# Performance work log

Measured on AMD Instinct MI355X. Metric: run time of the kernel, lower is better.

## Reference

```python
import jax, jax.numpy as jnp
import numpy as np

B, T, N, P, L = 8, 96, 20000, 12, 3
D = 32          # d_model (forced by channel-count identity d_model+96 == 4*d_model)
C = 4 * D       # 128 channels inside the linearized conv layers
M = 64          # random_feature_dim
TAU = 0.25
EPS = 1e-6      # numerical_stabilizer in random_feature_map


def _proj_matrix(m, d, seed=0):
    # create_random_matrix: stacked transposed-Q blocks from QR of gaussian blocks,
    # scaled row-wise by norms of a gaussian matrix (scaling=0).
    rng = np.random.RandomState(seed)
    blocks = []
    n_full = m // d
    for _ in range(n_full):
        q, _ = np.linalg.qr(rng.randn(d, d))
        blocks.append(q.T)
    rem = m - n_full * d
    if rem:
        q, _ = np.linalg.qr(rng.randn(d, d))
        blocks.append(q.T[:rem])
    mat = np.vstack(blocks)
    mult = np.linalg.norm(rng.randn(m, d), axis=1)
    return jnp.asarray(mult[:, None] * mat, dtype=jnp.float32)


def setup_inputs() -> dict:
    key = jax.random.key(0)
    ks = jax.random.split(key, 12)
    g = lambda k, shape, s=0.05: jax.random.normal(k, shape, jnp.float32) * s
    return {
        "x": jax.random.normal(ks[0], (B, T, N), jnp.float32),
        "x_mark": jax.random.uniform(ks[1], (B, T, 2), dtype=jnp.float32),
        "node_emb": g(ks[2], (N, D), 0.1),
        "time_tab": g(ks[3], (T, D), 0.1),
        "week_tab": g(ks[4], (7, D), 0.1),
        "input_w": g(ks[5], (D, 3 * T)),
        "input_b": jnp.zeros((D,), jnp.float32),
        "w1_w": g(ks[6], (D, 3 * D)),
        "w1_b": jnp.zeros((D,), jnp.float32),
        "w2_w": g(ks[7], (D, 3 * D)),
        "w2_b": jnp.zeros((D,), jnp.float32),
        "in_w": g(ks[8], (L, C, C)),
        "in_b": jnp.zeros((L, C), jnp.float32),
        "out_w": g(ks[9], (L, C, C)),
        "out_b": jnp.zeros((L, C), jnp.float32),
        "ln_g": jnp.ones((L, C), jnp.float32),
        "ln_b": jnp.zeros((L, C), jnp.float32),
        "reg_w": g(ks[10], (P, 2 * C)),
        "reg_b": jnp.zeros((P,), jnp.float32),
        "proj": _proj_matrix(M, D, seed=0),
    }


def _rfm(data, proj, is_query):
    # FAVOR+ positive random features (head dim == 1 folded out; shapes are [B,N,d])
    d = data.shape[-1]
    data = data * (float(d) ** -0.25)            # h(x) normalizer d^{-1/4}
    ratio = 1.0 / np.sqrt(float(proj.shape[0]))
    dash = jnp.einsum('bnd,md->bnm', data, proj)
    diag = 0.5 * jnp.sum(data * data, axis=-1, keepdims=True)
    if is_query:
        stab = jnp.max(dash, axis=-1, keepdims=True)          # per-row max
    else:
        stab = jnp.max(dash, axis=(1, 2), keepdims=True)      # max over features AND nodes
    return ratio * (jnp.exp(dash - diag - stab) + EPS)


def _linear_kernel(v, phi_q, phi_k):
    # associativity trick: (phi_q (phi_k^T v)) / (phi_q (phi_k^T 1))
    kv = jnp.einsum('bnm,bnc->bmc', phi_k, v)
    num = jnp.einsum('bnm,bmc->bnc', phi_q, kv)
    den = jnp.einsum('bnm,bm->bn', phi_q, jnp.sum(phi_k, axis=1))
    return num / den[..., None]


def reference(x, x_mark, node_emb, time_tab, week_tab, input_w, input_b,
              w1_w, w1_b, w2_w, w2_b, in_w, in_b, out_w, out_b,
              ln_g, ln_b, reg_w, reg_b, proj):
    Bq, Tq, Nq = x.shape
    marks = jax.lax.stop_gradient(x_mark)
    tod_idx = jnp.clip((marks[:, -1, 0] * Tq).astype(jnp.int32), 0, Tq - 1)
    dow_idx = jnp.clip((marks[:, -1, 1] * 7.0).astype(jnp.int32), 0, 6)
    time_e = jnp.broadcast_to(time_tab[tod_idx][:, None, :], (Bq, Nq, D))
    week_e = jnp.broadcast_to(week_tab[dow_idx][:, None, :], (Bq, Nq, D))
    node_e = jnp.broadcast_to(node_emb[None], (Bq, Nq, D))

    # input embedding over the flattened (feature-major) [3*T] channel axis
    tod_f = jnp.broadcast_to(x_mark[:, :, 0:1], (Bq, Tq, Nq))
    dow_f = jnp.broadcast_to(x_mark[:, :, 1:2], (Bq, Tq, Nq))
    feat = jnp.concatenate([x, tod_f, dow_f], axis=1)          # (B, 3T, N)
    x_in = jnp.einsum('bkn,ck->bnc', feat, input_w) + input_b  # (B, N, D)

    xg = jnp.concatenate([node_e, time_e, week_e], axis=-1)        # (B,N,3D)
    h = jnp.concatenate([x_in, node_e, time_e, week_e], axis=-1)   # (B,N,4D)

    inv_sqrt_tau = 1.0 / np.sqrt(TAU)
    nv1 = (jnp.einsum('bng,cg->bnc', xg, w1_w) + w1_b) * inv_sqrt_tau
    nv2 = (jnp.einsum('bng,cg->bnc', xg, w2_w) + w2_b) * inv_sqrt_tau
    # same node vectors (hence same data-derived seed / projection) every layer
    phi_q = _rfm(nv1, proj, True)    # (B,N,M)
    phi_k = _rfm(nv2, proj, False)   # (B,N,M)

    skip = h
    for i in range(L):
        res = h
        u = jax.nn.sigmoid(h @ in_w[i].T + in_b[i]) * (h @ out_w[i].T + out_b[i])
        u = _linear_kernel(u, phi_q, phi_k)
        h = u + res
        mu = jnp.mean(h, axis=-1, keepdims=True)
        var = jnp.var(h, axis=-1, keepdims=True)
        h = (h - mu) * jax.lax.rsqrt(var + 1e-5) * ln_g[i] + ln_b[i]

    out = jnp.concatenate([skip, h], axis=-1) @ reg_w.T + reg_b  # (B,N,P)
    return jnp.swapaxes(out, 1, 2)                               # (B,P,N)
```

## Files before the change

### kernel.cpp

```cpp
#include <hip/hip_runtime.h>

typedef unsigned short u16;
typedef __attribute__((ext_vector_type(8))) __bf16 bf16x8;
typedef __attribute__((ext_vector_type(4))) float f32x4;

#define BB 8
#define TT 96
#define NN 20000
#define NP 20224
#define PP 12
#define LL 3
#define DD 32
#define CC 128
#define MM 64
#define NB3 105
#define NB5 313
#define NB1 313

constexpr float KSC  = 0.8408964152537145f;
constexpr float KSC2 = 0.7071067811865476f;

__device__ inline u16 f2bf(float f){
  unsigned u = __float_as_uint(f);
  u = (u + 0x7fffu + ((u >> 16) & 1u)) >> 16;
  return (u16)u;
}
__device__ inline float bf2f(u16 h){ return __uint_as_float(((unsigned)h) << 16); }
__device__ inline unsigned fmapu(float f){
  unsigned u = __float_as_uint(f);
  return (u & 0x80000000u) ? ~u : (u | 0x80000000u);
}
__device__ inline float funmap(unsigned u){
  return (u & 0x80000000u) ? __uint_as_float(u & 0x7fffffffu) : __uint_as_float(~u);
}
__device__ inline unsigned pk2(float a, float b){
  return (unsigned)f2bf(a) | ((unsigned)f2bf(b) << 16);
}

__global__ void k0_prep(const float* xm, const float* time_tab, const float* week_tab,
                        const float* w1w, const float* w1b, const float* w2w, const float* w2b,
                        const float* inw, const float* inb, const float* proj,
                        float* bv1, float* bv2, float* sbd1, float* sbd2,
                        float* bc1, float* bc2, float* mb, int* tod, int* dow,
                        unsigned* cmx, float* ksum, float* qmat, float* emat)
{
  __shared__ float sT[BB][DD], sWk[BB][DD];
  __shared__ float sB1[BB][DD], sB2[BB][DD];
  __shared__ float sW1G[DD][DD], sW2G[DD][DD], sPJ[MM][DD];
  __shared__ int sTod[BB], sDow[BB];
  int tid = threadIdx.x;
  ksum[tid] = 0.f;
  for (int i = tid; i < DD*DD; i += 512){
    int c = i >> 5, g = i & 31;
    sW1G[c][g] = w1w[c*96 + g];
    sW2G[c][g] = w2w[c*96 + g];
  }
  for (int i = tid; i < MM*DD; i += 512) sPJ[i >> 5][i & 31] = proj[i];
  if (tid < BB){
    float t0 = xm[(tid*TT + TT-1)*2 + 0];
    float t1 = xm[(tid*TT + TT-1)*2 + 1];
    int ti = (int)(t0 * (float)TT); ti = min(max(ti, 0), TT-1);
    int di = (int)(t1 * 7.0f);      di = min(max(di, 0), 6);
    sTod[tid] = ti; sDow[tid] = di; tod[tid] = ti; dow[tid] = di;
  }
  if (tid < MM) cmx[tid] = fmapu(-3e38f);
  __syncthreads();
  if (tid < BB*DD){
    int b = tid >> 5, g = tid & 31;
    sT[b][g]  = time_tab[sTod[b]*DD + g];
    sWk[b][g] = week_tab[sDow[b]*DD + g];
  }
  __syncthreads();
  {
    int which = tid >> 8, b = (tid >> 5) & 7, c = tid & 31;
    const float* w  = which ? w2w : w1w;
    const float* wb = which ? w2b : w1b;
    float s = wb[c];
    for (int g = 0; g < DD; g++)
      s += sT[b][g]*w[c*96 + 32 + g] + sWk[b][g]*w[c*96 + 64 + g];
    if (which){ bv2[b*DD+c] = s; sB2[b][c] = s; }
    else      { bv1[b*DD+c] = s; sB1[b][c] = s; }
  }
  __syncthreads();
  for (int e = tid; e < 2*DD*MM; e += 512){
    int set = e >> 11, g = (e >> 6) & 31, m = e & 63;
    float s = 0.f;
    if (set == 0){ for (int c = 0; c < DD; c++) s += sW1G[c][g]*sPJ[m][c]; }
    else         { for (int c = 0; c < DD; c++) s += sW2G[c][g]*sPJ[m][c]; }
    qmat[e] = KSC * s;
  }
  {
    int set = tid >> 8, g = (tid >> 3) & 31, b = tid & 7;
    float s = 0.f;
    if (set == 0){ for (int c = 0; c < DD; c++) s += sW1G[c][g]*sB1[b][c]; }
    else         { for (int c = 0; c < DD; c++) s += sW2G[c][g]*sB2[b][c]; }
    emat[tid] = KSC2 * s;
  }
  {
    int b = tid >> 6, m = tid & 63;
    float s1 = 0.f, s2 = 0.f;
    for (int c = 0; c < DD; c++){
      float p = sPJ[m][c];
      s1 += sB1[b][c]*p; s2 += sB2[b][c]*p;
    }
    sbd1[b*MM+m] = KSC * s1;
    sbd2[b*MM+m] = KSC * s2;
  }
  if (tid < 16){
    int b = tid & 7;
    float s = 0.f;
    if (tid >> 3){ for (int c = 0; c < DD; c++) s += sB2[b][c]*sB2[b][c]; bc2[b] = 0.5f*KSC2*s; }
    else         { for (int c = 0; c < DD; c++) s += sB1[b][c]*sB1[b][c]; bc1[b] = 0.5f*KSC2*s; }
  }
  if (tid < 256){
    int b = tid >> 5, c = tid & 31;
    float s = inb[c];
    for (int t = 0; t < TT; t++){
      float m0 = xm[(b*TT+t)*2+0], m1 = xm[(b*TT+t)*2+1];
      s += m0 * inw[c*288 + 96 + t] + m1 * inw[c*288 + 192 + t];
    }
    mb[b*DD+c] = s;
  }
}

__global__ __launch_bounds__(256) void k1_node(
    const float* node_emb, const float* w1w, const float* w2w,
    const float* qmat, const float* emat,
    const float* gin_w, const float* gout_w,
    float* sd1, float* sd2, float* sq1, float* sq2,
    float* cr1, float* cr2, unsigned* cmx,
    u16* wbf, float* kvz)
{
  __shared__ float sQ1[DD*MM], sQ2[DD*MM];
  __shared__ float sW1[DD*DD], sW2[DD*DD];
  __shared__ float sE[2*DD*BB];
  __shared__ unsigned sCM[MM];
  int tid = threadIdx.x;
  int gid = blockIdx.x*256 + tid;
  const int TOT = NB1*256;
  for (int i = gid; i < LL*BB*MM*CC; i += TOT) kvz[i] = 0.f;
  for (int i = gid; i < 2*LL*CC*CC; i += TOT){
    int which = i / (LL*CC*CC);
    int r = i - which*(LL*CC*CC);
    wbf[i] = f2bf((which ? gout_w : gin_w)[r]);
  }
  for (int i = tid; i < DD*MM; i += 256){ sQ1[i] = qmat[i]; sQ2[i] = qmat[DD*MM + i]; }
  for (int i = tid; i < DD*DD; i += 256){
    sW1[i] = w1w[(i>>5)*96 + (i&31)];
    sW2[i] = w2w[(i>>5)*96 + (i&31)];
  }
  for (int i = tid; i < 2*DD*BB; i += 256) sE[i] = emat[i];
  if (tid < MM) sCM[tid] = fmapu(-3e38f);
  __syncthreads();
  int r = tid >> 2, q = tid & 3;
  int n = blockIdx.x*64 + r;
  bool valid = n < NN;
  int nc = valid ? n : 0;
  float nd[DD];
  #pragma unroll
  for (int g = 0; g < DD; g += 4){
    float4 v = *(const float4*)&node_emb[nc*DD + g];
    nd[g] = v.x; nd[g+1] = v.y; nd[g+2] = v.z; nd[g+3] = v.w;
  }
  float s1v[16], s2v[16];
  #pragma unroll
  for (int j = 0; j < 16; j++){ s1v[j] = 0.f; s2v[j] = 0.f; }
  #pragma unroll
  for (int g = 0; g < DD; g++){
    float xg = nd[g];
    #pragma unroll
    for (int jj = 0; jj < 16; jj += 4){
      float4 a1 = *(const float4*)&sQ1[g*MM + q*16 + jj];
      float4 a2 = *(const float4*)&sQ2[g*MM + q*16 + jj];
      s1v[jj+0] += xg*a1.x; s1v[jj+1] += xg*a1.y; s1v[jj+2] += xg*a1.z; s1v[jj+3] += xg*a1.w;
      s2v[jj+0] += xg*a2.x; s2v[jj+1] += xg*a2.y; s2v[jj+2] += xg*a2.z; s2v[jj+3] += xg*a2.w;
    }
  }
  if (valid){
    #pragma unroll
    for (int jj = 0; jj < 16; jj += 4){
      *(float4*)&sd1[(size_t)n*MM + q*16 + jj] = make_float4(s1v[jj], s1v[jj+1], s1v[jj+2], s1v[jj+3]);
      *(float4*)&sd2[(size_t)n*MM + q*16 + jj] = make_float4(s2v[jj], s2v[jj+1], s2v[jj+2], s2v[jj+3]);
    }
    #pragma unroll
    for (int j = 0; j < 16; j++)
      atomicMax(&sCM[q*16 + j], fmapu(s2v[j]));
  }
  float sqp1 = 0.f, sqp2 = 0.f;
  #pragma unroll
  for (int c8 = 0; c8 < 8; c8++){
    int c = q*8 + c8;
    float d1 = 0.f, d2 = 0.f;
    #pragma unroll
    for (int g = 0; g < DD; g += 4){
      float4 w1v = *(const float4*)&sW1[c*DD + g];
      float4 w2v = *(const float4*)&sW2[c*DD + g];
      d1 += nd[g]*w1v.x + nd[g+1]*w1v.y + nd[g+2]*w1v.z + nd[g+3]*w1v.w;
      d2 += nd[g]*w2v.x + nd[g+1]*w2v.y + nd[g+2]*w2v.z + nd[g+3]*w2v.w;
    }
    sqp1 += d1*d1; sqp2 += d2*d2;
  }
  sqp1 += __shfl_xor(sqp1, 1); sqp1 += __shfl_xor(sqp1, 2);
  sqp2 += __shfl_xor(sqp2, 1); sqp2 += __shfl_xor(sqp2, 2);
  if (q == 0 && valid){
    sq1[n] = 0.5f*KSC2*sqp1;
    sq2[n] = 0.5f*KSC2*sqp2;
  }
  {
    float cA1 = 0.f, cB1 = 0.f, cA2 = 0.f, cB2 = 0.f;
    #pragma unroll
    for (int g = 0; g < DD; g++){
      float xg = nd[g];
      cA1 += xg*sE[g*8 + 2*q];
      cB1 += xg*sE[g*8 + 2*q + 1];
      cA2 += xg*sE[256 + g*8 + 2*q];
      cB2 += xg*sE[256 + g*8 + 2*q + 1];
    }
    if (valid){
      cr1[(2*q)*NN + n]     = cA1;
      cr1[(2*q+1)*NN + n]   = cB1;
      cr2[(2*q)*NN + n]     = cA2;
      cr2[(2*q+1)*NN + n]   = cB2;
    }
  }
  __syncthreads();
  if (tid < MM) atomicMax(&cmx[tid], sCM[tid]);
}

__global__ void k0b_stab(const unsigned* cmx, const float* sbd2, float* stab){
  int lane = threadIdx.x;
  float cm = funmap(cmx[lane]);
  for (int b = 0; b < BB; b++){
    float v = cm + sbd2[b*MM + lane];
    #pragma unroll
    for (int off = 32; off; off >>= 1) v = fmaxf(v, __shfl_xor(v, off));
    if (lane == 0) stab[b] = v;
  }
}

__global__ __launch_bounds__(256) void k1b_phi(
    const float* sd1, const float* sd2, const float* sq1, const float* sq2,
    const float* cr1, const float* cr2, const float* sbd1, const float* sbd2,
    const float* bc1, const float* bc2, const float* stab,
    u16* phiq, u16* phikt, float* ksum)
{
  __shared__ u16 sT[MM][264];
  __shared__ float sQb[MM], sKb[MM];
  __shared__ float sRed[256];
  int tid = threadIdx.x;
  int b = blockIdx.y, n0 = blockIdx.x*256;
  if (tid < MM){
    sQb[tid] = sbd1[b*MM + tid];
    sKb[tid] = sbd2[b*MM + tid] - bc2[b] - stab[b];
  }
  __syncthreads();
  int n = n0 + tid;
  bool v = n < NN;
  int nc = v ? n : 0;
  float dq[MM];
  const float* s1r = sd1 + (size_t)nc*MM;
  #pragma unroll
  for (int m = 0; m < MM; m += 4){
    float4 t = *(const float4*)&s1r[m];
    dq[m]=t.x; dq[m+1]=t.y; dq[m+2]=t.z; dq[m+3]=t.w;
  }
  float rm = -3e38f;
  #pragma unroll
  for (int m = 0; m < MM; m++) rm = fmaxf(rm, dq[m] + sQb[m]);
  float diagq = sq1[nc] + cr1[b*NN + nc] + bc1[b];
  u16* pqr = phiq + ((size_t)(b*NN) + nc)*MM;
  #pragma unroll
  for (int m = 0; m < MM; m += 8){
    float p[8];
    #pragma unroll
    for (int j = 0; j < 8; j++){
      float ev = dq[m+j] + sQb[m+j] - rm - diagq;
      p[j] = 0.125f*__expf(ev) + 1.25e-7f;
    }
    uint4 w = { pk2(p[0],p[1]), pk2(p[2],p[3]), pk2(p[4],p[5]), pk2(p[6],p[7]) };
    if (v) *(uint4*)&pqr[m] = w;
  }
  const float* s2r = sd2 + (size_t)nc*MM;
  float diagk = sq2[nc] + cr2[b*NN + nc];
  #pragma unroll
  for (int m = 0; m < MM; m++){
    float ev = s2r[m] + sKb[m] - diagk;
    float pv = v ? (0.125f*__expf(ev) + 1.25e-7f) : 0.f;
    sT[m][tid] = f2bf(pv);
  }
  __syncthreads();
  {
    int m = tid >> 2, q = tid & 3;
    float s = 0.f;
    for (int j = 0; j < 64; j++) s += bf2f(sT[m][q*64 + j]);
    sRed[tid] = s;
  }
  __syncthreads();
  if (tid < MM){
    float s = sRed[tid*4] + sRed[tid*4+1] + sRed[tid*4+2] + sRed[tid*4+3];
    atomicAdd(&ksum[b*MM + tid], s);
  }
  {
    int m = tid >> 2, q = tid & 3;
    int nb = n0 + q*64;
    u16* dst = phikt + (size_t)(b*MM + m)*NP + nb;
    #pragma unroll
    for (int j = 0; j < 64; j += 8)
      *(uint4*)&dst[j] = *(const uint4*)&sT[m][q*64 + j];
  }
}

__global__ __launch_bounds__(256) void k2_embed(
    const float* x, const float* node_emb, const float* time_tab, const float* week_tab,
    const float* inw, const float* mb, const int* tod, const int* dow,
    u16* skip)
{
  __shared__ float sWt[TT*DD];
  __shared__ float sMB[DD], sTE[DD], sWE[DD];
  int tid = threadIdx.x;
  int b = blockIdx.y;
  for (int i = tid; i < TT*DD; i += 256){
    int t = i >> 5, c = i & 31;
    sWt[i] = inw[c*288 + t];
  }
  if (tid < DD){
    sMB[tid] = mb[b*DD + tid];
    sTE[tid] = time_tab[tod[b]*DD + tid];
    sWE[tid] = week_tab[dow[b]*DD + tid];
  }
  __syncthreads();
  int n = blockIdx.x*256 + tid;
  bool valid = n < NN;
  int nc = valid ? n : 0;
  float acc[DD];
  #pragma unroll
  for (int c = 0; c < DD; c++) acc[c] = sMB[c];
  const float* xb = x + (size_t)b*TT*NN + nc;
  for (int t = 0; t < TT; t++){
    float xv = xb[(size_t)t*NN];
    #pragma unroll
    for (int c = 0; c < DD; c++) acc[c] += xv * sWt[t*DD + c];
  }
  if (!valid) return;
  float nodev[DD];
  #pragma unroll
  for (int g = 0; g < DD; g += 4){
    float4 v = *(const float4*)&node_emb[n*DD + g];
    nodev[g] = v.x; nodev[g+1] = v.y; nodev[g+2] = v.z; nodev[g+3] = v.w;
  }
  auto chv = [&](int c)->float{
    if (c < 32)  return acc[c];
    if (c < 64)  return nodev[c-32];
    if (c < 96)  return sTE[c-64];
    return sWE[c-96];
  };
  u16* dst = skip + (size_t)(b*NN + n)*CC;
  #pragma unroll
  for (int g = 0; g < CC; g += 8){
    uint4 w;
    w.x = pk2(chv(g+0), chv(g+1));
    w.y = pk2(chv(g+2), chv(g+3));
    w.z = pk2(chv(g+4), chv(g+5));
    w.w = pk2(chv(g+6), chv(g+7));
    *(uint4*)&dst[g] = w;
  }
}

__global__ __launch_bounds__(256,2) void k3_gate(
    const u16* hin, const u16* wbf, const float* inb, const float* outb,
    const u16* phikt, float* kv, int layer)
{
  __shared__ u16 sUT[4][32*72];
  int tid = threadIdx.x;
  int b = blockIdx.y, blk = blockIdx.x;
  int lane = tid & 63, wave = tid >> 6, quad = lane >> 4, l15 = lane & 15;
  u16* myUT = &sUT[wave][0];

  float bi[2], bo[2];
  #pragma unroll
  for (int nt = 0; nt < 2; nt++){
    int co = wave*32 + nt*16 + l15;
    bi[nt] = inb[layer*CC + co];
    bo[nt] = outb[layer*CC + co];
  }
  bf16x8 bw[4][4];
  #pragma unroll
  for (int nt = 0; nt < 4; nt++){
    int which = nt >> 1;
    int co = wave*32 + (nt & 1)*16 + l15;
    const u16* wp = wbf + ((size_t)(which*LL + layer)*CC + co)*CC;
    #pragma unroll
    for (int ks = 0; ks < 4; ks++)
      bw[ks][nt] = *(const bf16x8*)&wp[ks*32 + quad*8];
  }
  f32x4 kvacc[4][2] = {};
  const u16* hbase = hin + (size_t)(b*NN)*CC;

  for (int ch = 0; ch < 3; ch++){
    int n0 = blk*192 + ch*64;
    f32x4 acc[4][4] = {};
    #pragma unroll
    for (int ks = 0; ks < 4; ks++){
      bf16x8 a[4];
      #pragma unroll
      for (int mt = 0; mt < 4; mt++)
        a[mt] = *(const bf16x8*)&hbase[(size_t)(n0 + mt*16 + l15)*CC + ks*32 + quad*8];
      #pragma unroll
      for (int mt = 0; mt < 4; mt++)
        #pragma unroll
        for (int nt = 0; nt < 4; nt++)
          acc[mt][nt] = __builtin_amdgcn_mfma_f32_16x16x32_bf16(a[mt], bw[ks][nt], acc[mt][nt], 0, 0, 0);
    }
    #pragma unroll
    for (int mt = 0; mt < 4; mt++){
      int r0 = mt*16 + quad*4;
      #pragma unroll
      for (int nt = 0; nt < 2; nt++){
        int cop = nt*16 + l15;
        float uv[4];
        #pragma unroll
        for (int e = 0; e < 4; e++){
          float up = acc[mt][nt][e] + bi[nt];
          float vp = acc[mt][nt+2][e] + bo[nt];
          float u = vp / (1.f + __expf(-up));
          if (n0 + r0 + e >= NN) u = 0.f;
          uv[e] = u;
        }
        ushort4 hv4;
        hv4.x = f2bf(uv[0]); hv4.y = f2bf(uv[1]); hv4.z = f2bf(uv[2]); hv4.w = f2bf(uv[3]);
        *(ushort4*)&myUT[cop*72 + r0] = hv4;
      }
    }
    #pragma unroll
    for (int ks2 = 0; ks2 < 2; ks2++){
      bf16x8 ap[4], bu[2];
      #pragma unroll
      for (int mtp = 0; mtp < 4; mtp++)
        ap[mtp] = *(const bf16x8*)&phikt[(size_t)(b*MM + mtp*16 + l15)*NP + n0 + ks2*32 + quad*8];
      #pragma unroll
      for (int nt2 = 0; nt2 < 2; nt2++)
        bu[nt2] = *(const bf16x8*)&myUT[(nt2*16 + l15)*72 + ks2*32 + quad*8];
      #pragma unroll
      for (int mtp = 0; mtp < 4; mtp++)
        #pragma unroll
        for (int nt2 = 0; nt2 < 2; nt2++)
          kvacc[mtp][nt2] = __builtin_amdgcn_mfma_f32_16x16x32_bf16(ap[mtp], bu[nt2], kvacc[mtp][nt2], 0, 0, 0);
    }
  }
  float* kvb = kv + (size_t)(layer*BB + b)*MM*CC;
  #pragma unroll
  for (int mt = 0; mt < 4; mt++)
    #pragma unroll
    for (int nt2 = 0; nt2 < 2; nt2++)
      #pragma unroll
      for (int e = 0; e < 4; e++)
        atomicAdd(&kvb[(mt*16 + quad*4 + e)*CC + wave*32 + nt2*16 + l15], kvacc[mt][nt2][e]);
}

__global__ void k4_reduce(const float* kv, const float* ksum, u16* kvt, int layer){
  int b = blockIdx.x;
  int tid = threadIdx.x;
  const float* kvb = kv + (size_t)(layer*BB + b)*MM*CC;
  for (int idx = tid; idx < 144*MM; idx += 256){
    int c = idx >> 6, m = idx & 63;
    float v = (c < CC) ? kvb[m*CC + c] : ((c == CC) ? ksum[b*MM + m] : 0.f);
    kvt[(size_t)b*144*MM + idx] = f2bf(v);
  }
}

__global__ __launch_bounds__(256,2) void k53(
    const u16* hin, u16* hout, const u16* phiq, const u16* kvt,
    const float* lng, const float* lnb,
    const u16* wbf, const float* g_inb, const float* g_outb, const u16* phikt,
    float* kv, int lat, int lgt)
{
  __shared__ u16 sH[64*136];
  __shared__ u16 sUT[4][32*72];
  int tid = threadIdx.x;
  int b = blockIdx.y, blk = blockIdx.x;
  int lane = tid & 63, wave = tid >> 6, quad = lane >> 4, l15 = lane & 15;
  u16* myUT = &sUT[wave][0];
  const u16* kvb = kvt + (size_t)b*144*MM;
  float lg[8], lb[8];
  #pragma unroll
  for (int nt = 0; nt < 8; nt++){
    lg[nt] = lng[lat*CC + nt*16 + l15];
    lb[nt] = lnb[lat*CC + nt*16 + l15];
  }
  float bi[2], bo[2];
  #pragma unroll
  for (int p = 0; p < 2; p++){
    int co = wave*32 + p*16 + l15;
    bi[p] = g_inb[lgt*CC + co];
    bo[p] = g_outb[lgt*CC + co];
  }
  bf16x8 bw[4][4];
  #pragma unroll
  for (int nt = 0; nt < 4; nt++){
    int which = nt >> 1;
    int co = wave*32 + (nt & 1)*16 + l15;
    const u16* wp = wbf + ((size_t)(which*LL + lgt)*CC + co)*CC;
    #pragma unroll
    for (int ks = 0; ks < 4; ks++)
      bw[ks][nt] = *(const bf16x8*)&wp[ks*32 + quad*8];
  }
  f32x4 kvacc[4][2] = {};
  const u16* hb_in = hin + (size_t)(b*NN)*CC;
  u16* hb_out = hout + (size_t)(b*NN)*CC;

  for (int ch = 0; ch < 3; ch++){
    int n0 = blk*192 + ch*64;
    {
      int r = wave*16 + (lane >> 2), seg = lane & 3;
      int n = n0 + r;
      const u16* src = hb_in + (size_t)min(n, NN-1)*CC + seg*32;
      #pragma unroll
      for (int k = 0; k < 32; k += 8){
        uint4 d = *(const uint4*)&src[k];
        *(uint2*)&sH[r*136 + seg*32 + k]     = make_uint2(d.x, d.y);
        *(uint2*)&sH[r*136 + seg*32 + k + 4] = make_uint2(d.z, d.w);
      }
    }
    bf16x8 aq[2];
    #pragma unroll
    for (int ks = 0; ks < 2; ks++)
      aq[ks] = *(const bf16x8*)&phiq[((size_t)(b*NN) + n0 + wave*16 + l15)*MM + ks*32 + quad*8];
    f32x4 nacc[9] = {};
    #pragma unroll
    for (int ks = 0; ks < 2; ks++)
      #pragma unroll
      for (int nt = 0; nt < 9; nt++){
        bf16x8 bk = *(const bf16x8*)&kvb[(nt*16 + l15)*MM + ks*32 + quad*8];
        nacc[nt] = __builtin_amdgcn_mfma_f32_16x16x32_bf16(aq[ks], bk, nacc[nt], 0, 0, 0);
      }
    #pragma unroll
    for (int e = 0; e < 4; e++){
      float den = __shfl(nacc[8][e], lane & 48);
      int rml = wave*16 + quad*4 + e;
      float y[8];
      float s1 = 0.f, s2 = 0.f;
      #pragma unroll
      for (int nt = 0; nt < 8; nt++){
        float res = bf2f(sH[rml*136 + nt*16 + l15]);
        float yv = nacc[nt][e]/den + res;
        y[nt] = yv; s1 += yv; s2 += yv*yv;
      }
      #pragma unroll
      for (int off = 1; off < 16; off <<= 1){
        s1 += __shfl_xor(s1, off);
        s2 += __shfl_xor(s2, off);
      }
      float mu = s1 * (1.f/CC);
      float rs = rsqrtf(s2 * (1.f/CC) - mu*mu + 1e-5f);
      #pragma unroll
      for (int nt = 0; nt < 8; nt++){
        int c = nt*16 + l15;
        sH[rml*136 + c] = f2bf((y[nt] - mu)*rs*lg[nt] + lb[nt]);
      }
    }
    {
      int r = wave*16 + (lane >> 2), seg = lane & 3;
      int n = n0 + r;
      if (n < NN){
        u16* dst = hb_out + (size_t)n*CC + seg*32;
        #pragma unroll
        for (int k = 0; k < 32; k += 8){
          uint2 a = *(const uint2*)&sH[r*136 + seg*32 + k];
          uint2 c2 = *(const uint2*)&sH[r*136 + seg*32 + k + 4];
          uint4 w = { a.x, a.y, c2.x, c2.y };
          *(uint4*)&dst[k] = w;
        }
      }
    }
    __syncthreads();
    f32x4 accm[4][4] = {};
    #pragma unroll
    for (int ks = 0; ks < 4; ks++){
      bf16x8 a[4];
      #pragma unroll
      for (int mt = 0; mt < 4; mt++)
        a[mt] = *(const bf16x8*)&sH[(mt*16 + l15)*136 + ks*32 + quad*8];
      #pragma unroll
      for (int mt = 0; mt < 4; mt++)
        #pragma unroll
        for (int nt = 0; nt < 4; nt++)
          accm[mt][nt] = __builtin_amdgcn_mfma_f32_16x16x32_bf16(a[mt], bw[ks][nt], accm[mt][nt], 0, 0, 0);
    }
    #pragma unroll
    for (int mt = 0; mt < 4; mt++){
      int r0 = mt*16 + quad*4;
      #pragma unroll
      for (int nt = 0; nt < 2; nt++){
        float uv[4];
        #pragma unroll
        for (int e = 0; e < 4; e++){
          float up = accm[mt][nt][e] + bi[nt];
          float vp = accm[mt][nt+2][e] + bo[nt];
          float u = vp / (1.f + __expf(-up));
          if (n0 + r0 + e >= NN) u = 0.f;
          uv[e] = u;
        }
        ushort4 hv4;
        hv4.x = f2bf(uv[0]); hv4.y = f2bf(uv[1]); hv4.z = f2bf(uv[2]); hv4.w = f2bf(uv[3]);
        *(ushort4*)&myUT[(nt*16 + l15)*72 + r0] = hv4;
      }
    }
    #pragma unroll
    for (int ks2 = 0; ks2 < 2; ks2++){
      bf16x8 ap[4], bu2[2];
      #pragma unroll
      for (int mtp = 0; mtp < 4; mtp++)
        ap[mtp] = *(const bf16x8*)&phikt[(size_t)(b*MM + mtp*16 + l15)*NP + n0 + ks2*32 + quad*8];
      #pragma unroll
      for (int nt2 = 0; nt2 < 2; nt2++)
        bu2[nt2] = *(const bf16x8*)&myUT[(nt2*16 + l15)*72 + ks2*32 + quad*8];
      #pragma unroll
      for (int mtp = 0; mtp < 4; mtp++)
        #pragma unroll
        for (int nt2 = 0; nt2 < 2; nt2++)
          kvacc[mtp][nt2] = __builtin_amdgcn_mfma_f32_16x16x32_bf16(ap[mtp], bu2[nt2], kvacc[mtp][nt2], 0, 0, 0);
    }
    __syncthreads();
  }
  float* kvw = kv + (size_t)(lgt*BB + b)*MM*CC;
  #pragma unroll
  for (int mt = 0; mt < 4; mt++)
    #pragma unroll
    for (int nt2 = 0; nt2 < 2; nt2++)
      #pragma unroll
      for (int e = 0; e < 4; e++)
        atomicAdd(&kvw[(mt*16 + quad*4 + e)*CC + wave*32 + nt2*16 + l15], kvacc[mt][nt2][e]);
}

__global__ __launch_bounds__(256) void k5_attn(
    const u16* hin, u16* hout, const u16* phiq, const u16* kvt,
    const float* lng, const float* lnb, int layer)
{
  __shared__ u16 sH[64*132];
  int tid = threadIdx.x;
  int b = blockIdx.y, n0 = blockIdx.x*64;
  int lane = tid & 63, wave = tid >> 6, quad = lane >> 4, l15 = lane & 15;
  const u16* kvb = kvt + (size_t)b*144*MM;
  {
    int r = wave*16 + (lane >> 2), seg = lane & 3;
    int n = n0 + r;
    const u16* src = hin + (size_t)(b*NN + min(n, NN-1))*CC + seg*32;
    #pragma unroll
    for (int k = 0; k < 32; k += 8){
      uint4 d = *(const uint4*)&src[k];
      *(uint2*)&sH[r*132 + seg*32 + k]     = make_uint2(d.x, d.y);
      *(uint2*)&sH[r*132 + seg*32 + k + 4] = make_uint2(d.z, d.w);
    }
  }
  bf16x8 aq[2];
  #pragma unroll
  for (int ks = 0; ks < 2; ks++)
    aq[ks] = *(const bf16x8*)&phiq[((size_t)(b*NN) + n0 + wave*16 + l15)*MM + ks*32 + quad*8];
  f32x4 nacc[9] = {};
  #pragma unroll
  for (int ks = 0; ks < 2; ks++)
    #pragma unroll
    for (int nt = 0; nt < 9; nt++){
      bf16x8 bk = *(const bf16x8*)&kvb[(nt*16 + l15)*MM + ks*32 + quad*8];
      nacc[nt] = __builtin_amdgcn_mfma_f32_16x16x32_bf16(aq[ks], bk, nacc[nt], 0, 0, 0);
    }
  float lg[8], lb[8];
  #pragma unroll
  for (int nt = 0; nt < 8; nt++){
    lg[nt] = lng[layer*CC + nt*16 + l15];
    lb[nt] = lnb[layer*CC + nt*16 + l15];
  }
  #pragma unroll
  for (int e = 0; e < 4; e++){
    float den = __shfl(nacc[8][e], lane & 48);
    int rml = wave*16 + quad*4 + e;
    float y[8];
    float s1 = 0.f, s2 = 0.f;
    #pragma unroll
    for (int nt = 0; nt < 8; nt++){
      float res = bf2f(sH[rml*132 + nt*16 + l15]);
      float yv = nacc[nt][e]/den + res;
      y[nt] = yv; s1 += yv; s2 += yv*yv;
    }
    #pragma unroll
    for (int off = 1; off < 16; off <<= 1){
      s1 += __shfl_xor(s1, off);
      s2 += __shfl_xor(s2, off);
    }
    float mu = s1 * (1.f/CC);
    float rs = rsqrtf(s2 * (1.f/CC) - mu*mu + 1e-5f);
    #pragma unroll
    for (int nt = 0; nt < 8; nt++){
      int c = nt*16 + l15;
      sH[rml*132 + c] = f2bf((y[nt] - mu)*rs*lg[nt] + lb[nt]);
    }
  }
  {
    int r = wave*16 + (lane >> 2), seg = lane & 3;
    int n = n0 + r;
    if (n < NN){
      u16* dst = hout + (size_t)(b*NN + n)*CC + seg*32;
      #pragma unroll
      for (int k = 0; k < 32; k += 8){
        uint2 a = *(const uint2*)&sH[r*132 + seg*32 + k];
        uint2 c2 = *(const uint2*)&sH[r*132 + seg*32 + k + 4];
        uint4 w = { a.x, a.y, c2.x, c2.y };
        *(uint4*)&dst[k] = w;
      }
    }
  }
}

__global__ __launch_bounds__(256) void k6_final(
    const u16* skip, const u16* hbuf, const float* regw, const float* regb,
    float* out)
{
  __shared__ float sRW[PP*256];
  __shared__ float sRB[PP];
  int tid = threadIdx.x;
  for (int i = tid; i < PP*256; i += 256) sRW[i] = regw[i];
  if (tid < PP) sRB[tid] = regb[tid];
  __syncthreads();
  int b = blockIdx.y;
  int n = blockIdx.x*256 + tid;
  if (n >= NN) return;
  float acc[PP];
  #pragma unroll
  for (int p = 0; p < PP; p++) acc[p] = sRB[p];
  const u16* sr = skip + (size_t)(b*NN + n)*CC;
  const u16* hr = hbuf + (size_t)(b*NN + n)*CC;
  for (int half = 0; half < 2; half++){
    const u16* src = half ? hr : sr;
    int coff = half*128;
    for (int k = 0; k < CC; k += 8){
      uint4 d = *(const uint4*)&src[k];
      float v0 = __uint_as_float(d.x<<16), v1 = __uint_as_float(d.x & 0xffff0000u);
      float v2 = __uint_as_float(d.y<<16), v3 = __uint_as_float(d.y & 0xffff0000u);
      float v4 = __uint_as_float(d.z<<16), v5 = __uint_as_float(d.z & 0xffff0000u);
      float v6 = __uint_as_float(d.w<<16), v7 = __uint_as_float(d.w & 0xffff0000u);
      #pragma unroll
      for (int p = 0; p < PP; p++){
        const float* wr = &sRW[p*256 + coff + k];
        acc[p] += v0*wr[0] + v1*wr[1] + v2*wr[2] + v3*wr[3]
                + v4*wr[4] + v5*wr[5] + v6*wr[6] + v7*wr[7];
      }
    }
  }
  #pragma unroll
  for (int p = 0; p < PP; p++)
    out[(size_t)(b*PP + p)*NN + n] = acc[p];
}

extern "C" void kernel_launch(void* const* d_in, const int* in_sizes, int n_in,
                              void* d_out, int out_size, void* d_ws, size_t ws_size,
                              hipStream_t stream)
{
  const float* x        = (const float*)d_in[0];
  const float* xm       = (const float*)d_in[1];
  const float* node_emb = (const float*)d_in[2];
  const float* time_tab = (const float*)d_in[3];
  const float* week_tab = (const float*)d_in[4];
  const float* input_w  = (const float*)d_in[5];
  const float* input_b  = (const float*)d_in[6];
  const float* w1w      = (const float*)d_in[7];
  const float* w1b      = (const float*)d_in[8];
  const float* w2w      = (const float*)d_in[9];
  const float* w2b      = (const float*)d_in[10];
  const float* inw      = (const float*)d_in[11];
  const float* inb      = (const float*)d_in[12];
  const float* outw     = (const float*)d_in[13];
  const float* outb     = (const float*)d_in[14];
  const float* lng      = (const float*)d_in[15];
  const float* lnb      = (const float*)d_in[16];
  const float* regw     = (const float*)d_in[17];
  const float* regb     = (const float*)d_in[18];
  const float* proj     = (const float*)d_in[19];
  float* out = (float*)d_out;

  char* wsb = (char*)d_ws;
  size_t off = 0;
  auto alloc = [&](size_t bytes)->char*{
    char* p = wsb + off; off += (bytes + 255) & ~(size_t)255; return p;
  };
  u16*   skip  = (u16*)  alloc((size_t)BB*NN*CC*2);
  u16*   hbuf  = (u16*)  alloc((size_t)BB*NN*CC*2);
  u16*   phiq  = (u16*)  alloc((size_t)BB*NN*MM*2);
  u16*   phikt = (u16*)  alloc((size_t)BB*MM*NP*2 + 4096);
  float* sd1   = (float*)alloc((size_t)NN*MM*4);
  float* sd2   = (float*)alloc((size_t)NN*MM*4);
  float* sq1   = (float*)alloc((size_t)NN*4);
  float* sq2   = (float*)alloc((size_t)NN*4);
  float* cr1   = (float*)alloc((size_t)BB*NN*4);
  float* cr2   = (float*)alloc((size_t)BB*NN*4);
  u16*   wbf   = (u16*)  alloc((size_t)2*LL*CC*CC*2);
  float* kv    = (float*)alloc((size_t)LL*BB*MM*CC*4);
  u16*   kvt   = (u16*)  alloc((size_t)BB*144*MM*2);
  float* ksum  = (float*)alloc(BB*MM*4);
  float* bv1   = (float*)alloc(BB*DD*4);
  float* bv2   = (float*)alloc(BB*DD*4);
  float* sbd1  = (float*)alloc(BB*MM*4);
  float* sbd2  = (float*)alloc(BB*MM*4);
  float* bc1   = (float*)alloc(BB*4);
  float* bc2   = (float*)alloc(BB*4);
  float* mb    = (float*)alloc(BB*DD*4);
  int*   tod   = (int*)  alloc(BB*4);
  int*   dow   = (int*)  alloc(BB*4);
  unsigned* cmx= (unsigned*)alloc(MM*4);
  float* stab  = (float*)alloc(BB*4);
  float* qmat  = (float*)alloc(2*DD*MM*4);
  float* emat  = (float*)alloc(2*DD*BB*4);
  (void)ws_size; (void)in_sizes; (void)n_in; (void)out_size;

  k0_prep<<<1, 512, 0, stream>>>(xm, time_tab, week_tab, w1w, w1b, w2w, w2b,
                                 input_w, input_b, proj,
                                 bv1, bv2, sbd1, sbd2, bc1, bc2, mb, tod, dow, cmx, ksum,
                                 qmat, emat);
  k1_node<<<NB1, 256, 0, stream>>>(node_emb, w1w, w2w, qmat, emat, inw, outw,
                                   sd1, sd2, sq1, sq2, cr1, cr2, cmx, wbf, kv);
  k0b_stab<<<1, 64, 0, stream>>>(cmx, sbd2, stab);
  k1b_phi<<<dim3(79, 8), 256, 0, stream>>>(sd1, sd2, sq1, sq2, cr1, cr2,
                                           sbd1, sbd2, bc1, bc2, stab,
                                           phiq, phikt, ksum);
  k2_embed<<<dim3(79, 8), 256, 0, stream>>>(x, node_emb, time_tab, week_tab,
                                            input_w, mb, tod, dow, skip);
  k3_gate<<<dim3(NB3, 8), 256, 0, stream>>>(skip, wbf, inb, outb, phikt, kv, 0);
  k4_reduce<<<8, 256, 0, stream>>>(kv, ksum, kvt, 0);
  k53<<<dim3(NB3, 8), 256, 0, stream>>>(skip, hbuf, phiq, kvt, lng, lnb,
                                        wbf, inb, outb, phikt, kv, 0, 1);
  k4_reduce<<<8, 256, 0, stream>>>(kv, ksum, kvt, 1);
  k53<<<dim3(NB3, 8), 256, 0, stream>>>(hbuf, hbuf, phiq, kvt, lng, lnb,
                                        wbf, inb, outb, phikt, kv, 1, 2);
  k4_reduce<<<8, 256, 0, stream>>>(kv, ksum, kvt, 2);
  k5_attn<<<dim3(NB5, 8), 256, 0, stream>>>(hbuf, hbuf, phiq, kvt, lng, lnb, 2);
  k6_final<<<dim3(79, 8), 256, 0, stream>>>(skip, hbuf, regw, regb, out);
}
```

Baseline: 702.9 us.

## Cut register pressure in gate kernels to raise occupancy; unroll input projection

The gate GEMMs in k3_gate and k53 no longer keep all weight fragments and the 4x4 accumulator tile in registers. They now loop over two 16-column halves, reloading weight fragments from global memory each chunk and reading biases and LayerNorm parameters on demand. Launch bounds go from 2 to 3 blocks per CU. The input-projection time loop is unrolled by four to expose more independent loads. The trade is more global and cache traffic for weights and params, and activation tiles reread twice, in exchange for higher occupancy.

```diff
diff --git a/kernel.cpp b/kernel.cpp
--- a/kernel.cpp
+++ b/kernel.cpp
@@ -336,10 +336,18 @@
   #pragma unroll
   for (int c = 0; c < DD; c++) acc[c] = sMB[c];
   const float* xb = x + (size_t)b*TT*NN + nc;
-  for (int t = 0; t < TT; t++){
-    float xv = xb[(size_t)t*NN];
-    #pragma unroll
-    for (int c = 0; c < DD; c++) acc[c] += xv * sWt[t*DD + c];
+  for (int t = 0; t < TT; t += 4){
+    float xv0 = xb[(size_t)(t+0)*NN];
+    float xv1 = xb[(size_t)(t+1)*NN];
+    float xv2 = xb[(size_t)(t+2)*NN];
+    float xv3 = xb[(size_t)(t+3)*NN];
+    #pragma unroll
+    for (int c = 0; c < DD; c++){
+      acc[c] += xv0 * sWt[(t+0)*DD + c];
+      acc[c] += xv1 * sWt[(t+1)*DD + c];
+      acc[c] += xv2 * sWt[(t+2)*DD + c];
+      acc[c] += xv3 * sWt[(t+3)*DD + c];
+    }
   }
   if (!valid) return;
   float nodev[DD];
@@ -366,7 +374,7 @@
   }
 }
 
-__global__ __launch_bounds__(256,2) void k3_gate(
+__global__ __launch_bounds__(256,3) void k3_gate(
     const u16* hin, const u16* wbf, const float* inb, const float* outb,
     const u16* phikt, float* kv, int layer)
 {
@@ -375,76 +383,60 @@
   int b = blockIdx.y, blk = blockIdx.x;
   int lane = tid & 63, wave = tid >> 6, quad = lane >> 4, l15 = lane & 15;
   u16* myUT = &sUT[wave][0];
-
-  float bi[2], bo[2];
-  #pragma unroll
-  for (int nt = 0; nt < 2; nt++){
-    int co = wave*32 + nt*16 + l15;
-    bi[nt] = inb[layer*CC + co];
-    bo[nt] = outb[layer*CC + co];
-  }
-  bf16x8 bw[4][4];
-  #pragma unroll
-  for (int nt = 0; nt < 4; nt++){
-    int which = nt >> 1;
-    int co = wave*32 + (nt & 1)*16 + l15;
-    const u16* wp = wbf + ((size_t)(which*LL + layer)*CC + co)*CC;
-    #pragma unroll
-    for (int ks = 0; ks < 4; ks++)
-      bw[ks][nt] = *(const bf16x8*)&wp[ks*32 + quad*8];
-  }
+  const u16* wub = wbf + ((size_t)(0*LL + layer)*CC)*CC;
+  const u16* wvb = wbf + ((size_t)(1*LL + layer)*CC)*CC;
+  const u16* hbase = hin + (size_t)(b*NN)*CC;
   f32x4 kvacc[4][2] = {};
-  const u16* hbase = hin + (size_t)(b*NN)*CC;
 
   for (int ch = 0; ch < 3; ch++){
     int n0 = blk*192 + ch*64;
-    f32x4 acc[4][4] = {};
-    #pragma unroll
-    for (int ks = 0; ks < 4; ks++){
-      bf16x8 a[4];
-      #pragma unroll
-      for (int mt = 0; mt < 4; mt++)
-        a[mt] = *(const bf16x8*)&hbase[(size_t)(n0 + mt*16 + l15)*CC + ks*32 + quad*8];
-      #pragma unroll
-      for (int mt = 0; mt < 4; mt++)
+    #pragma unroll
+    for (int p = 0; p < 2; p++){
+      int co = wave*32 + p*16 + l15;
+      f32x4 accu[4] = {}, accv[4] = {};
+      #pragma unroll
+      for (int ks = 0; ks < 4; ks++){
+        bf16x8 bu = *(const bf16x8*)&wub[(size_t)co*CC + ks*32 + quad*8];
+        bf16x8 bv = *(const bf16x8*)&wvb[(size_t)co*CC + ks*32 + quad*8];
         #pragma unroll
-        for (int nt = 0; nt < 4; nt++)
-          acc[mt][nt] = __builtin_amdgcn_mfma_f32_16x16x32_bf16(a[mt], bw[ks][nt], acc[mt][nt], 0, 0, 0);
-    }
-    #pragma unroll
-    for (int mt = 0; mt < 4; mt++){
-      int r0 = mt*16 + quad*4;
-      #pragma unroll
-      for (int nt = 0; nt < 2; nt++){
-        int cop = nt*16 + l15;
+        for (int mt = 0; mt < 4; mt++){
+          bf16x8 a = *(const bf16x8*)&hbase[(size_t)(n0 + mt*16 + l15)*CC + ks*32 + quad*8];
+          accu[mt] = __builtin_amdgcn_mfma_f32_16x16x32_bf16(a, bu, accu[mt], 0, 0, 0);
+          accv[mt] = __builtin_amdgcn_mfma_f32_16x16x32_bf16(a, bv, accv[mt], 0, 0, 0);
+        }
+      }
+      float bi = inb[layer*CC + co], bo = outb[layer*CC + co];
+      #pragma unroll
+      for (int mt = 0; mt < 4; mt++){
+        int r0 = mt*16 + quad*4;
         float uv[4];
         #pragma unroll
         for (int e = 0; e < 4; e++){
-          float up = acc[mt][nt][e] + bi[nt];
-          float vp = acc[mt][nt+2][e] + bo[nt];
+          float up = accu[mt][e] + bi;
+          float vp = accv[mt][e] + bo;
           float u = vp / (1.f + __expf(-up));
           if (n0 + r0 + e >= NN) u = 0.f;
           uv[e] = u;
         }
         ushort4 hv4;
         hv4.x = f2bf(uv[0]); hv4.y = f2bf(uv[1]); hv4.z = f2bf(uv[2]); hv4.w = f2bf(uv[3]);
-        *(ushort4*)&myUT[cop*72 + r0] = hv4;
+        *(ushort4*)&myUT[(p*16 + l15)*72 + r0] = hv4;
       }
     }
     #pragma unroll
     for (int ks2 = 0; ks2 < 2; ks2++){
-      bf16x8 ap[4], bu[2];
+      bf16x8 ap[4], bu2[2];
       #pragma unroll
       for (int mtp = 0; mtp < 4; mtp++)
         ap[mtp] = *(const bf16x8*)&phikt[(size_t)(b*MM + mtp*16 + l15)*NP + n0 + ks2*32 + quad*8];
       #pragma unroll
       for (int nt2 = 0; nt2 < 2; nt2++)
-        bu[nt2] = *(const bf16x8*)&myUT[(nt2*16 + l15)*72 + ks2*32 + quad*8];
+        bu2[nt2] = *(const bf16x8*)&myUT[(nt2*16 + l15)*72 + ks2*32 + quad*8];
       #pragma unroll
       for (int mtp = 0; mtp < 4; mtp++)
         #pragma unroll
         for (int nt2 = 0; nt2 < 2; nt2++)
-          kvacc[mtp][nt2] = __builtin_amdgcn_mfma_f32_16x16x32_bf16(ap[mtp], bu[nt2], kvacc[mtp][nt2], 0, 0, 0);
+          kvacc[mtp][nt2] = __builtin_amdgcn_mfma_f32_16x16x32_bf16(ap[mtp], bu2[nt2], kvacc[mtp][nt2], 0, 0, 0);
     }
   }
   float* kvb = kv + (size_t)(layer*BB + b)*MM*CC;
@@ -468,7 +460,7 @@
   }
 }
 
-__global__ __launch_bounds__(256,2) void k53(
+__global__ __launch_bounds__(256,3) void k53(
     const u16* hin, u16* hout, const u16* phiq, const u16* kvt,
     const float* lng, const float* lnb,
     const u16* wbf, const float* g_inb, const float* g_outb, const u16* phikt,
@@ -481,29 +473,6 @@
   int lane = tid & 63, wave = tid >> 6, quad = lane >> 4, l15 = lane & 15;
   u16* myUT = &sUT[wave][0];
   const u16* kvb = kvt + (size_t)b*144*MM;
-  float lg[8], lb[8];
-  #pragma unroll
-  for (int nt = 0; nt < 8; nt++){
-    lg[nt] = lng[lat*CC + nt*16 + l15];
-    lb[nt] = lnb[lat*CC + nt*16 + l15];
-  }
-  float bi[2], bo[2];
-  #pragma unroll
-  for (int p = 0; p < 2; p++){
-    int co = wave*32 + p*16 + l15;
-    bi[p] = g_inb[lgt*CC + co];
-    bo[p] = g_outb[lgt*CC + co];
-  }
-  bf16x8 bw[4][4];
-  #pragma unroll
-  for (int nt = 0; nt < 4; nt++){
-    int which = nt >> 1;
-    int co = wave*32 + (nt & 1)*16 + l15;
-    const u16* wp = wbf + ((size_t)(which*LL + lgt)*CC + co)*CC;
-    #pragma unroll
-    for (int ks = 0; ks < 4; ks++)
-      bw[ks][nt] = *(const bf16x8*)&wp[ks*32 + quad*8];
-  }
   f32x4 kvacc[4][2] = {};
   const u16* hb_in = hin + (size_t)(b*NN)*CC;
   u16* hb_out = hout + (size_t)(b*NN)*CC;
@@ -555,7 +524,7 @@
       #pragma unroll
       for (int nt = 0; nt < 8; nt++){
         int c = nt*16 + l15;
-        sH[rml*136 + c] = f2bf((y[nt] - mu)*rs*lg[nt] + lb[nt]);
+        sH[rml*136 + c] = f2bf((y[nt] - mu)*rs*lng[lat*CC + c] + lnb[lat*CC + c]);
       }
     }
     {
@@ -573,36 +542,39 @@
       }
     }
     __syncthreads();
-    f32x4 accm[4][4] = {};
-    #pragma unroll
-    for (int ks = 0; ks < 4; ks++){
-      bf16x8 a[4];
-      #pragma unroll
-      for (int mt = 0; mt < 4; mt++)
-        a[mt] = *(const bf16x8*)&sH[(mt*16 + l15)*136 + ks*32 + quad*8];
-      #pragma unroll
-      for (int mt = 0; mt < 4; mt++)
+    const u16* wub = wbf + ((size_t)(0*LL + lgt)*CC)*CC;
+    const u16* wvb = wbf + ((size_t)(1*LL + lgt)*CC)*CC;
+    #pragma unroll
+    for (int p = 0; p < 2; p++){
+      int co = wave*32 + p*16 + l15;
+      f32x4 accu[4] = {}, accv[4] = {};
+      #pragma unroll
+      for (int ks = 0; ks < 4; ks++){
+        bf16x8 bu = *(const bf16x8*)&wub[(size_t)co*CC + ks*32 + quad*8];
+        bf16x8 bv = *(const bf16x8*)&wvb[(size_t)co*CC + ks*32 + quad*8];
         #pragma unroll
-        for (int nt = 0; nt < 4; nt++)
-          accm[mt][nt] = __builtin_amdgcn_mfma_f32_16x16x32_bf16(a[mt], bw[ks][nt], accm[mt][nt], 0, 0, 0);
-    }
-    #pragma unroll
-    for (int mt = 0; mt < 4; mt++){
-      int r0 = mt*16 + quad*4;
-      #pragma unroll
-      for (int nt = 0; nt < 2; nt++){
+        for (int mt = 0; mt < 4; mt++){
+          bf16x8 a = *(const bf16x8*)&sH[(mt*16 + l15)*136 + ks*32 + quad*8];
+          accu[mt] = __builtin_amdgcn_mfma_f32_16x16x32_bf16(a, bu, accu[mt], 0, 0, 0);
+          accv[mt] = __builtin_amdgcn_mfma_f32_16x16x32_bf16(a, bv, accv[mt], 0, 0, 0);
+        }
+      }
+      float bi = g_inb[lgt*CC + co], bo = g_outb[lgt*CC + co];
+      #pragma unroll
+      for (int mt = 0; mt < 4; mt++){
+        int r0 = mt*16 + quad*4;
         float uv[4];
         #pragma unroll
         for (int e = 0; e < 4; e++){
-          float up = accm[mt][nt][e] + bi[nt];
-          float vp = accm[mt][nt+2][e] + bo[nt];
+          float up = accu[mt][e] + bi;
+          float vp = accv[mt][e] + bo;
           float u = vp / (1.f + __expf(-up));
           if (n0 + r0 + e >= NN) u = 0.f;
           uv[e] = u;
         }
         ushort4 hv4;
         hv4.x = f2bf(uv[0]); hv4.y = f2bf(uv[1]); hv4.z = f2bf(uv[2]); hv4.w = f2bf(uv[3]);
-        *(ushort4*)&myUT[(nt*16 + l15)*72 + r0] = hv4;
+        *(ushort4*)&myUT[(p*16 + l15)*72 + r0] = hv4;
       }
     }
     #pragma unroll
```

After: 738.8 us. 5.1% more time.
